# Optimization experiments

Measured on AMD Instinct MI355X. Metric: run time of the kernel, lower is better.

The kernel has to match this reference:

```python
import jax, jax.numpy as jnp
import numpy as np


def _quantize(m):
    # per-row symmetric int8 quantization: absmax over last dim, round to nearest-even
    max_val = jnp.max(jnp.abs(m), axis=-1)          # [...]
    q = jnp.round(m * (127.0 / max_val)[..., None])  # values in [-127, 127], kept in fp32
    return q, max_val


def setup_inputs() -> dict:
    key = jax.random.key(0)
    k1, k2, k3 = jax.random.split(key, 3)
    B, S, D_IN, D_OUT = 4, 8192, 1024, 1024
    x = jax.random.normal(k1, (B, S, D_IN), dtype=jnp.float32)
    weight = jax.random.normal(k2, (D_OUT, D_IN), dtype=jnp.float32) * 0.02
    bias = jax.random.normal(k3, (D_OUT,), dtype=jnp.float32)
    return {"x": x, "weight": weight, "bias": bias}


def reference(x, weight, bias):
    # weight quantization happens once in __init__; replicated here for self-containment
    w_q, w_max = _quantize(weight)    # [N,K], [N]
    x_q, x_max = _quantize(x)         # [B,S,K], [B,S]
    # int8 GEMM emulated in fp32, exactly as the original module does
    res_q = jnp.einsum('bsk,nk->bsn', x_q, w_q)            # [B,S,N] fp32
    mx = x_max[..., None] * w_max                          # outer-product dequant scale [B,S,N]
    res = (res_q / (127.0 * 127.0)).astype(jnp.float16) * mx  # fp16 * fp32 -> fp32
    return res + bias
```

## Files before the change

kernel.cpp:

```cpp
#include <hip/hip_runtime.h>
#include <hip/hip_fp16.h>


typedef int i32x4 __attribute__((ext_vector_type(4)));

#define BM 128
#define BN 128
#define KB 64

__global__ __launch_bounds__(256) void quant_rows_kernel(
    const float* __restrict__ in, signed char* __restrict__ q,
    float* __restrict__ rowmax, int K, int R) {
  const int row = blockIdx.x;
  const int t = threadIdx.x;
  const size_t base = (size_t)row * K;
  float4 v = reinterpret_cast<const float4*>(in + base)[t];
  float a = fmaxf(fmaxf(fabsf(v.x), fabsf(v.y)), fmaxf(fabsf(v.z), fabsf(v.w)));
#pragma unroll
  for (int off = 32; off > 0; off >>= 1) a = fmaxf(a, __shfl_xor(a, off, 64));
  __shared__ float smax[4];
  if ((t & 63) == 0) smax[t >> 6] = a;
  __syncthreads();
  float m = fmaxf(fmaxf(smax[0], smax[1]), fmaxf(smax[2], smax[3]));
  float s = 127.0f / m;
  char4 qq;
  qq.x = (signed char)(int)rintf(v.x * s);
  qq.y = (signed char)(int)rintf(v.y * s);
  qq.z = (signed char)(int)rintf(v.z * s);
  qq.w = (signed char)(int)rintf(v.w * s);
  const int kb = t >> 4;
  signed char* dst = q + (size_t)kb * R * KB + (size_t)row * KB + (t & 15) * 4;
  *reinterpret_cast<char4*>(dst) = qq;
  if (t == 0) rowmax[row] = m;
}

__device__ __forceinline__ void gload_lds16(const void* g, void* l) {
  __builtin_amdgcn_global_load_lds(
      (const __attribute__((address_space(1))) unsigned char*)g,
      (__attribute__((address_space(3))) unsigned char*)l, 16, 0, 0);
}

__global__ __launch_bounds__(256, 4) void w8x8_gemm_kernel(
    const signed char* __restrict__ Aq, const signed char* __restrict__ Bq,
    const float* __restrict__ Amax, const float* __restrict__ Bmax,
    const float* __restrict__ bias, float* __restrict__ out,
    int M, int N, int K, int cpx) {
  __shared__ __align__(16) signed char ldsA[2][BM * KB];
  __shared__ __align__(16) signed char ldsB[2][BN * KB];
  const int t = threadIdx.x;
  const int lane = t & 63;
  const int wave = t >> 6;
  const int wrow = wave >> 1, wcol = wave & 1;

  const int nbn = N / BN;
  const int bid = blockIdx.x;
  const int tile = (bid & 7) * cpx + (bid >> 3);
  const int bm = tile / nbn, bn = tile % nbn;

  const size_t kbA = (size_t)M * KB;
  const size_t kbB = (size_t)N * KB;
  const signed char* Abase = Aq + (size_t)bm * BM * KB;
  const signed char* Bbase = Bq + (size_t)bn * BN * KB;

  const int rS = t >> 2;
  const int gs0 = (rS << 6) | ((((t & 3) ^ ((rS >> 1) & 3))) << 4);
  const int dst0 = t * 16;

  const int fr = lane & 15, fq = lane >> 4;
  const int pcs = (fq ^ ((fr >> 1) & 3)) << 4;
  int aoff[4], boff[4];
#pragma unroll
  for (int m = 0; m < 4; ++m) {
    aoff[m] = (wrow * 64 + m * 16 + fr) * KB + pcs;
    boff[m] = (wcol * 64 + m * 16 + fr) * KB + pcs;
  }

  i32x4 acc[4][4];
#pragma unroll
  for (int m = 0; m < 4; ++m)
#pragma unroll
    for (int n = 0; n < 4; ++n) acc[m][n] = (i32x4){0, 0, 0, 0};

#define STAGE(bf, kt)                                                  \
  do {                                                                 \
    const signed char* ga = Abase + (size_t)(kt) * kbA + gs0;          \
    const signed char* gb = Bbase + (size_t)(kt) * kbB + gs0;          \
    gload_lds16(ga, &ldsA[bf][dst0]);                                  \
    gload_lds16(ga + 4096, &ldsA[bf][dst0 + 4096]);                    \
    gload_lds16(gb, &ldsB[bf][dst0]);                                  \
    gload_lds16(gb + 4096, &ldsB[bf][dst0 + 4096]);                    \
  } while (0)

  const int NT = K / KB;
  STAGE(0, 0);

  for (int kt = 0; kt < NT; ++kt) {
    const bool pf = (kt + 1 < NT);
    if (pf) STAGE((kt + 1) & 1, kt + 1);
    if (pf)
      asm volatile("s_waitcnt vmcnt(4)" ::: "memory");
    else
      asm volatile("s_waitcnt vmcnt(0)" ::: "memory");
    __builtin_amdgcn_s_barrier();

    const signed char* lA = ldsA[kt & 1];
    const signed char* lB = ldsB[kt & 1];
    i32x4 a[4], b[4];
#pragma unroll
    for (int m = 0; m < 4; ++m) {
      a[m] = *reinterpret_cast<const i32x4*>(lA + aoff[m]);
      b[m] = *reinterpret_cast<const i32x4*>(lB + boff[m]);
    }
    __builtin_amdgcn_s_setprio(1);
#pragma unroll
    for (int m = 0; m < 4; ++m)
#pragma unroll
      for (int n = 0; n < 4; ++n)
        acc[m][n] = __builtin_amdgcn_mfma_i32_16x16x64_i8(a[m], b[n],
                                                          acc[m][n], 0, 0, 0);
    __builtin_amdgcn_s_setprio(0);

    if (pf) __builtin_amdgcn_s_barrier();
  }
#undef STAGE

  const int row0 = bm * BM + wrow * 64;
  const int col0 = bn * BN + wcol * 64;
  const float C = 1.0f / 16129.0f;
  float wmx[4], bs[4];
#pragma unroll
  for (int n = 0; n < 4; ++n) {
    int col = col0 + n * 16 + fr;
    wmx[n] = Bmax[col];
    bs[n] = bias[col];
  }
#pragma unroll
  for (int m = 0; m < 4; ++m) {
#pragma unroll
    for (int r = 0; r < 4; ++r) {
      int row = row0 + m * 16 + fq * 4 + r;
      float xm = Amax[row];
      float* orow = out + (size_t)row * N;
#pragma unroll
      for (int n = 0; n < 4; ++n) {
        float v = (float)acc[m][n][r] * C;
        float h = __half2float(__float2half_rn(v));
        orow[col0 + n * 16 + fr] = h * (xm * wmx[n]) + bs[n];
      }
    }
  }
}

extern "C" void kernel_launch(void* const* d_in, const int* in_sizes, int n_in,
                              void* d_out, int out_size, void* d_ws, size_t ws_size,
                              hipStream_t stream) {
  const float* x = (const float*)d_in[0];
  const float* w = (const float*)d_in[1];
  const float* bias = (const float*)d_in[2];
  float* out = (float*)d_out;

  const int N = in_sizes[2];
  const int K = in_sizes[1] / N;
  const int M = in_sizes[0] / K;

  signed char* xq = (signed char*)d_ws;
  signed char* wq = xq + (size_t)M * K;
  float* xmax = (float*)(wq + (size_t)N * K);
  float* wmax = xmax + M;

  quant_rows_kernel<<<M, 256, 0, stream>>>(x, xq, xmax, K, M);
  quant_rows_kernel<<<N, 256, 0, stream>>>(w, wq, wmax, K, N);

  const int nwg = (M / BM) * (N / BN);
  const int cpx = nwg / 8;
  w8x8_gemm_kernel<<<nwg, 256, 0, stream>>>(xq, wq, xmax, wmax, bias, out,
                                            M, N, K, cpx);
}
```

Baseline: 89.13 us.

## Load GEMM operands directly from global into registers, dropping LDS staging

Replaces the LDS double-buffered staging (global_load_lds plus barriers) with direct per-wave global loads of MFMA fragments into registers. Two register sets are ping-ponged across K tiles, and occupancy is lowered to 3 waves per SIMD to leave room for the extra registers. This removes the LDS traffic and barriers, but each wave now fetches its own copy of the shared A/B tiles from L2/global, so operand reuse across waves is lost. It also assumes NT is even.

```diff
diff --git a/kernel.cpp b/kernel.cpp
--- a/kernel.cpp
+++ b/kernel.cpp
@@ -34,19 +34,11 @@
   if (t == 0) rowmax[row] = m;
 }
 
-__device__ __forceinline__ void gload_lds16(const void* g, void* l) {
-  __builtin_amdgcn_global_load_lds(
-      (const __attribute__((address_space(1))) unsigned char*)g,
-      (__attribute__((address_space(3))) unsigned char*)l, 16, 0, 0);
-}
-
-__global__ __launch_bounds__(256, 4) void w8x8_gemm_kernel(
+__global__ __launch_bounds__(256, 3) void w8x8_gemm_kernel(
     const signed char* __restrict__ Aq, const signed char* __restrict__ Bq,
     const float* __restrict__ Amax, const float* __restrict__ Bmax,
     const float* __restrict__ bias, float* __restrict__ out,
     int M, int N, int K, int cpx) {
-  __shared__ __align__(16) signed char ldsA[2][BM * KB];
-  __shared__ __align__(16) signed char ldsB[2][BN * KB];
   const int t = threadIdx.x;
   const int lane = t & 63;
   const int wave = t >> 6;
@@ -59,21 +51,11 @@
 
   const size_t kbA = (size_t)M * KB;
   const size_t kbB = (size_t)N * KB;
-  const signed char* Abase = Aq + (size_t)bm * BM * KB;
-  const signed char* Bbase = Bq + (size_t)bn * BN * KB;
-
-  const int rS = t >> 2;
-  const int gs0 = (rS << 6) | ((((t & 3) ^ ((rS >> 1) & 3))) << 4);
-  const int dst0 = t * 16;
-
   const int fr = lane & 15, fq = lane >> 4;
-  const int pcs = (fq ^ ((fr >> 1) & 3)) << 4;
-  int aoff[4], boff[4];
-#pragma unroll
-  for (int m = 0; m < 4; ++m) {
-    aoff[m] = (wrow * 64 + m * 16 + fr) * KB + pcs;
-    boff[m] = (wcol * 64 + m * 16 + fr) * KB + pcs;
-  }
+  const signed char* pa =
+      Aq + (size_t)bm * BM * KB + ((wrow * 64 + fr) << 6) + (fq << 4);
+  const signed char* pb =
+      Bq + (size_t)bn * BN * KB + ((wcol * 64 + fr) << 6) + (fq << 4);
 
   i32x4 acc[4][4];
 #pragma unroll
@@ -81,48 +63,41 @@
 #pragma unroll
     for (int n = 0; n < 4; ++n) acc[m][n] = (i32x4){0, 0, 0, 0};
 
-#define STAGE(bf, kt)                                                  \
+#define LOADF(A_, B_, kt)                                              \
   do {                                                                 \
-    const signed char* ga = Abase + (size_t)(kt) * kbA + gs0;          \
-    const signed char* gb = Bbase + (size_t)(kt) * kbB + gs0;          \
-    gload_lds16(ga, &ldsA[bf][dst0]);                                  \
-    gload_lds16(ga + 4096, &ldsA[bf][dst0 + 4096]);                    \
-    gload_lds16(gb, &ldsB[bf][dst0]);                                  \
-    gload_lds16(gb + 4096, &ldsB[bf][dst0 + 4096]);                    \
+    const signed char* ga = pa + (size_t)(kt) * kbA;                   \
+    const signed char* gb = pb + (size_t)(kt) * kbB;                   \
+    A_[0] = *reinterpret_cast<const i32x4*>(ga);                       \
+    A_[1] = *reinterpret_cast<const i32x4*>(ga + 1024);                \
+    A_[2] = *reinterpret_cast<const i32x4*>(ga + 2048);                \
+    A_[3] = *reinterpret_cast<const i32x4*>(ga + 3072);                \
+    B_[0] = *reinterpret_cast<const i32x4*>(gb);                       \
+    B_[1] = *reinterpret_cast<const i32x4*>(gb + 1024);                \
+    B_[2] = *reinterpret_cast<const i32x4*>(gb + 2048);                \
+    B_[3] = *reinterpret_cast<const i32x4*>(gb + 3072);                \
+  } while (0)
+
+#define MFMA16(A_, B_)                                                   \
+  do {                                                                   \
+    __builtin_amdgcn_s_setprio(1);                                       \
+    _Pragma("unroll") for (int m = 0; m < 4; ++m)                        \
+        _Pragma("unroll") for (int n = 0; n < 4; ++n) acc[m][n] =        \
+        __builtin_amdgcn_mfma_i32_16x16x64_i8(A_[m], B_[n], acc[m][n],   \
+                                              0, 0, 0);                  \
+    __builtin_amdgcn_s_setprio(0);                                       \
   } while (0)
 
   const int NT = K / KB;
-  STAGE(0, 0);
-
-  for (int kt = 0; kt < NT; ++kt) {
-    const bool pf = (kt + 1 < NT);
-    if (pf) STAGE((kt + 1) & 1, kt + 1);
-    if (pf)
-      asm volatile("s_waitcnt vmcnt(4)" ::: "memory");
-    else
-      asm volatile("s_waitcnt vmcnt(0)" ::: "memory");
-    __builtin_amdgcn_s_barrier();
-
-    const signed char* lA = ldsA[kt & 1];
-    const signed char* lB = ldsB[kt & 1];
-    i32x4 a[4], b[4];
-#pragma unroll
-    for (int m = 0; m < 4; ++m) {
-      a[m] = *reinterpret_cast<const i32x4*>(lA + aoff[m]);
-      b[m] = *reinterpret_cast<const i32x4*>(lB + boff[m]);
-    }
-    __builtin_amdgcn_s_setprio(1);
-#pragma unroll
-    for (int m = 0; m < 4; ++m)
-#pragma unroll
-      for (int n = 0; n < 4; ++n)
-        acc[m][n] = __builtin_amdgcn_mfma_i32_16x16x64_i8(a[m], b[n],
-                                                          acc[m][n], 0, 0, 0);
-    __builtin_amdgcn_s_setprio(0);
-
-    if (pf) __builtin_amdgcn_s_barrier();
+  i32x4 a0[4], b0[4], a1[4], b1[4];
+  LOADF(a0, b0, 0);
+  for (int kt = 0; kt < NT; kt += 2) {
+    LOADF(a1, b1, kt + 1);
+    MFMA16(a0, b0);
+    if (kt + 2 < NT) LOADF(a0, b0, kt + 2);
+    MFMA16(a1, b1);
   }
-#undef STAGE
+#undef LOADF
+#undef MFMA16
 
   const int row0 = bm * BM + wrow * 64;
   const int col0 = bn * BN + wcol * 64;
```

New measurement: 111.1 us. 24.7% more time.
